# Kernel optimization log

Hardware: AMD Instinct MI355X
Metric: run time of the kernel (lower is better)

## Reference

```python
import jax, jax.numpy as jnp
import numpy as np

V, D, H, L, FF, C = 32000, 512, 8, 3, 2048, 6
B, S = 32, 1024


def setup_inputs() -> dict:
    key = jax.random.key(0)
    ks = jax.random.split(key, 8)
    tokens = jax.random.randint(ks[0], (B, S), 0, V, dtype=jnp.int32)
    emb = jax.random.normal(ks[1], (V, D), dtype=jnp.float32) * 0.02
    qkv_w = jax.random.normal(ks[2], (L, D, 3 * D), dtype=jnp.float32) * (D ** -0.5)
    qkv_b = jnp.zeros((L, 3 * D), dtype=jnp.float32)
    fc_w = jax.random.normal(ks[3], (L, D, D), dtype=jnp.float32) * (D ** -0.5)
    fc_b = jnp.zeros((L, D), dtype=jnp.float32)
    gamma = jnp.ones((D,), dtype=jnp.float32)
    beta = jnp.zeros((D,), dtype=jnp.float32)
    fc1_w = jax.random.normal(ks[4], (D, FF), dtype=jnp.float32) * (D ** -0.5)
    fc1_b = jnp.zeros((FF,), dtype=jnp.float32)
    fc2_w = jax.random.normal(ks[5], (FF, C), dtype=jnp.float32) * (FF ** -0.5)
    fc2_b = jnp.zeros((C,), dtype=jnp.float32)
    return dict(tokens=tokens, emb=emb, qkv_w=qkv_w, qkv_b=qkv_b, fc_w=fc_w,
                fc_b=fc_b, gamma=gamma, beta=beta, fc1_w=fc1_w, fc1_b=fc1_b,
                fc2_w=fc2_w, fc2_b=fc2_b)


def _sinusoidal_pe(seq_len, dim):
    pos = jnp.arange(seq_len, dtype=jnp.float32)[:, None]
    div = jnp.exp(jnp.arange(0, dim, 2).astype(jnp.float32) * (-np.log(10000.0) / dim))
    pe = jnp.zeros((seq_len, dim), dtype=jnp.float32)
    pe = pe.at[:, 0::2].set(jnp.sin(pos * div))
    pe = pe.at[:, 1::2].set(jnp.cos(pos * div))
    return pe


def reference(tokens, emb, qkv_w, qkv_b, fc_w, fc_b, gamma, beta, fc1_w, fc1_b, fc2_w, fc2_b):
    b, s = tokens.shape
    dh = D // H
    scale = dh ** -0.5

    def layernorm(y):
        m = y.mean(-1, keepdims=True)
        v = ((y - m) ** 2).mean(-1, keepdims=True)
        return (y - m) * jax.lax.rsqrt(v + 1e-5) * gamma + beta

    x = emb[tokens] + _sinusoidal_pe(s, D)[None]  # [B,S,D]
    for l in range(L):
        qkv = (x @ qkv_w[l] + qkv_b[l]).reshape(b, s, H, 3, dh)
        q = qkv[..., 0, :].transpose(0, 2, 1, 3)  # [B,H,S,dh]
        k = qkv[..., 1, :].transpose(0, 2, 1, 3)
        v = qkv[..., 2, :].transpose(0, 2, 1, 3)
        attn = jax.nn.softmax(jnp.einsum('bhqd,bhkd->bhqk', q, k) * scale, axis=-1)
        o = jnp.einsum('bhqk,bhkd->bhqd', attn, v).transpose(0, 2, 1, 3).reshape(b, s, D)
        o = o @ fc_w[l] + fc_b[l]
        x = layernorm(o + x)
    pooled = x.mean(axis=1)  # [B,D]
    h = jax.nn.relu(pooled @ fc1_w + fc1_b)  # dropout is identity at inference
    return h @ fc2_w + fc2_b
```

## Files before the change

### kernel.cpp

```cpp
#include <hip/hip_runtime.h>
#include <cmath>

#define BS_TOK 32768
#define DMODEL 512
#define NHEAD 8
#define DHEAD 64
#define NLAYER 3
#define FFDIM 2048
#define NCLS 6
#define BATCH 32
#define SEQ 1024
#define QKVW 1536

typedef short short8 __attribute__((ext_vector_type(8)));
typedef float float4v __attribute__((ext_vector_type(4)));
typedef unsigned int uint4v __attribute__((ext_vector_type(4)));
#define MFMA_BF16 __builtin_amdgcn_mfma_f32_16x16x32_bf16
#define QSCALE 0.18033688011112042f

__device__ __forceinline__ unsigned short f2bf(float x) {
    return (unsigned short)((__float_as_uint(x) + 0x8000u) >> 16);
}

__device__ __forceinline__ unsigned int cvt_pk_bf16(float a, float b) {
    unsigned int r;
    asm("v_cvt_pk_bf16_f32 %0, %1, %2" : "=v"(r) : "v"(a), "v"(b));
    return r;
}

#define PL32(a, b) asm("v_permlane32_swap_b32 %0, %1" : "+v"(a), "+v"(b))
#define PL16(a, b) asm("v_permlane16_swap_b32 %0, %1" : "+v"(a), "+v"(b))

__device__ __forceinline__ void gload16(const unsigned short* g, unsigned short* l) {
    __builtin_amdgcn_global_load_lds(
        (const __attribute__((address_space(1))) unsigned int*)g,
        (__attribute__((address_space(3))) unsigned int*)l, 16, 0, 0);
}

__global__ __launch_bounds__(128) void embed_pe_kernel(const int* __restrict__ tokens,
                                                       const float* __restrict__ emb,
                                                       float* __restrict__ X,
                                                       unsigned short* __restrict__ Xb) {
    int t = blockIdx.x;
    int pos = t & (SEQ - 1);
    int tok = tokens[t];
    int d0 = threadIdx.x * 4;
    float4 e = *(const float4*)(emb + (size_t)tok * DMODEL + d0);
    const float c = -9.210340371976184f / 512.0f;
    float div0 = expf((float)d0 * c);
    float div1 = expf((float)(d0 + 2) * c);
    float a0 = (float)pos * div0;
    float a1 = (float)pos * div1;
    e.x += sinf(a0); e.y += cosf(a0);
    e.z += sinf(a1); e.w += cosf(a1);
    *(float4*)(X + (size_t)t * DMODEL + d0) = e;
    *(ushort4*)(Xb + (size_t)t * DMODEL + d0) =
        make_ushort4(f2bf(e.x), f2bf(e.y), f2bf(e.z), f2bf(e.w));
}

__global__ __launch_bounds__(256) void transcvt_kernel(const float* __restrict__ in,
                                                       unsigned short* __restrict__ out,
                                                       int R, int C) {
    __shared__ float t[32][33];
    size_t base = (size_t)blockIdx.z * R * C;
    int c0 = blockIdx.x * 32, r0 = blockIdx.y * 32;
    int tx = threadIdx.x & 31, ty = threadIdx.x >> 5;
#pragma unroll
    for (int i = 0; i < 4; i++)
        t[ty + i * 8][tx] = in[base + (size_t)(r0 + ty + i * 8) * C + c0 + tx];
    __syncthreads();
#pragma unroll
    for (int i = 0; i < 4; i++)
        out[base + (size_t)(c0 + ty + i * 8) * R + r0 + tx] = f2bf(t[tx][ty + i * 8]);
}

__global__ __launch_bounds__(256) void transcvt_qkv_kernel(const float* __restrict__ in,
                                                           unsigned short* __restrict__ out) {
    __shared__ float t[32][33];
    int l = blockIdx.z;
    int n0 = blockIdx.x * 32, r0 = blockIdx.y * 32;
    int seg = n0 >> 9, nn = n0 & 511, h = nn >> 6, d0 = nn & 63;
    int c0 = h * 192 + seg * 64 + d0;
    float s = (seg == 0) ? QSCALE : 1.f;
    const float* inp = in + (size_t)l * DMODEL * QKVW;
    unsigned short* op = out + (size_t)l * QKVW * DMODEL;
    int tx = threadIdx.x & 31, ty = threadIdx.x >> 5;
#pragma unroll
    for (int i = 0; i < 4; i++)
        t[ty + i * 8][tx] = inp[(size_t)(r0 + ty + i * 8) * QKVW + c0 + tx];
    __syncthreads();
#pragma unroll
    for (int i = 0; i < 4; i++)
        op[(size_t)(n0 + ty + i * 8) * DMODEL + r0 + tx] = f2bf(t[tx][ty + i * 8] * s);
}

__global__ __launch_bounds__(256) void permbias_kernel(const float* __restrict__ qkv_b,
                                                       float* __restrict__ pb) {
    int i = blockIdx.x * 256 + threadIdx.x;
    int l = i / QKVW, n = i - l * QKVW;
    int seg = n >> 9, nn = n & 511, h = nn >> 6, d = nn & 63;
    float s = (seg == 0) ? QSCALE : 1.f;
    pb[i] = qkv_b[l * QKVW + h * 192 + seg * 64 + d] * s;
}

__global__ __launch_bounds__(256, 3) void gemm_qkv_kernel(const unsigned short* __restrict__ A,
                                                          const unsigned short* __restrict__ Bt,
                                                          const float* __restrict__ pb,
                                                          unsigned short* __restrict__ QKc,
                                                          unsigned short* __restrict__ Vt,
                                                          int M) {
    __shared__ unsigned short As[2][128 * 32];
    __shared__ unsigned short Bs[2][128 * 32];
    int bm = blockIdx.y * 128, bn = blockIdx.x * 128;
    int tid = threadIdx.x;
    int w = tid >> 6, lane = tid & 63, l15 = lane & 15, quad = lane >> 4;
    int wm = (w & 1) * 64, wn = (w >> 1) * 64;

    float4v acc[4][4];
    float4v z = {0.f, 0.f, 0.f, 0.f};
#pragma unroll
    for (int i = 0; i < 4; i++)
#pragma unroll
        for (int j = 0; j < 4; j++) acc[i][j] = z;

    int sr0 = w * 16 + (lane >> 2);
    int sr1 = (w + 4) * 16 + (lane >> 2);
    int sc = ((lane & 3) ^ ((lane >> 3) & 3)) * 8;
    const unsigned short* Ag = A + (size_t)bm * DMODEL;
    const unsigned short* Bg = Bt + (size_t)bn * DMODEL;

    gload16(Ag + (size_t)sr0 * DMODEL + sc, &As[0][w * 512]);
    gload16(Ag + (size_t)sr1 * DMODEL + sc, &As[0][(w + 4) * 512]);
    gload16(Bg + (size_t)sr0 * DMODEL + sc, &Bs[0][w * 512]);
    gload16(Bg + (size_t)sr1 * DMODEL + sc, &Bs[0][(w + 4) * 512]);
    __syncthreads();

    int sw = (l15 >> 1) & 3;
    for (int kt = 0; kt < 16; kt++) {
        const unsigned short* Ac = As[kt & 1];
        const unsigned short* Bc = Bs[kt & 1];
        if (kt + 1 < 16) {
            int kn = (kt + 1) * 32;
            unsigned short* An = (unsigned short*)As[(kt + 1) & 1];
            unsigned short* Bn = (unsigned short*)Bs[(kt + 1) & 1];
            gload16(Ag + (size_t)sr0 * DMODEL + kn + sc, &An[w * 512]);
            gload16(Ag + (size_t)sr1 * DMODEL + kn + sc, &An[(w + 4) * 512]);
            gload16(Bg + (size_t)sr0 * DMODEL + kn + sc, &Bn[w * 512]);
            gload16(Bg + (size_t)sr1 * DMODEL + kn + sc, &Bn[(w + 4) * 512]);
        }
        short8 af[4], bf[4];
#pragma unroll
        for (int i = 0; i < 4; i++)
            af[i] = *(short8*)&Ac[(wm + i * 16 + l15) * 32 + (quad ^ sw) * 8];
#pragma unroll
        for (int j = 0; j < 4; j++)
            bf[j] = *(short8*)&Bc[(wn + j * 16 + l15) * 32 + (quad ^ sw) * 8];
        __builtin_amdgcn_s_setprio(1);
#pragma unroll
        for (int i = 0; i < 4; i++)
#pragma unroll
            for (int j = 0; j < 4; j++)
                acc[i][j] = MFMA_BF16(af[i], bf[j], acc[i][j], 0, 0, 0);
        __builtin_amdgcn_s_setprio(0);
        __syncthreads();
    }

    float bj[4];
#pragma unroll
    for (int j = 0; j < 4; j++) bj[j] = pb[bn + wn + j * 16 + l15];

    if (bn < 1024) {
#pragma unroll
        for (int i = 0; i < 4; i++)
#pragma unroll
            for (int r = 0; r < 4; r++) {
                size_t row = (size_t)(bm + wm + i * 16 + quad * 4 + r);
#pragma unroll
                for (int j = 0; j < 4; j++)
                    QKc[row * 1024 + bn + wn + j * 16 + l15] = f2bf(acc[i][j][r] + bj[j]);
            }
    } else {
        int bl = bm >> 10;
        int sbase = (bm & 1023) + wm;
#pragma unroll
        for (int j = 0; j < 4; j++) {
            int colp = bn - 1024 + wn + j * 16 + l15;
            int h = colp >> 6, d = colp & 63;
            unsigned short* vb = Vt + ((size_t)(bl * 8 + h) * 64 + d) * 1024 + sbase;
#pragma unroll
            for (int i = 0; i < 4; i++) {
                ushort4 v4 = make_ushort4(f2bf(acc[i][j][0] + bj[j]),
                                          f2bf(acc[i][j][1] + bj[j]),
                                          f2bf(acc[i][j][2] + bj[j]),
                                          f2bf(acc[i][j][3] + bj[j]));
                *(ushort4*)(vb + i * 16 + quad * 4) = v4;
            }
        }
    }
}

__global__ __launch_bounds__(256, 2) void attn_kernel(const unsigned short* __restrict__ QKc,
                                                      const unsigned short* __restrict__ Vt,
                                                      unsigned short* __restrict__ O) {
    __shared__ unsigned short Ks[64 * 72];
    __shared__ unsigned short Vts[64 * 72];
    int bh = blockIdx.y;
    int b = bh >> 3, h = bh & 7;
    int q0 = blockIdx.x * 256;
    int tid = threadIdx.x;
    int w = tid >> 6, lane = tid & 63, l15 = lane & 15, quad = lane >> 4;
    const unsigned short* Kg = QKc + (size_t)b * SEQ * 1024 + 512 + h * 64;
    const unsigned short* Vg = Vt + (size_t)bh * 64 * 1024;

    short8 qf[4][2];
#pragma unroll
    for (int i = 0; i < 4; i++) {
        const unsigned short* qb =
            QKc + (size_t)(b * SEQ + q0 + w * 64 + i * 16 + l15) * 1024 + h * 64;
        qf[i][0] = *(const short8*)(qb + quad * 8);
        qf[i][1] = *(const short8*)(qb + 32 + quad * 8);
    }

    float lsum[4] = {0.f, 0.f, 0.f, 0.f};
    float4v accO[4][4];
    float4v z = {0.f, 0.f, 0.f, 0.f};
#pragma unroll
    for (int i = 0; i < 4; i++)
#pragma unroll
        for (int dc = 0; dc < 4; dc++) accO[i][dc] = z;

    int sr = tid >> 2, so = (tid & 3) * 16;

    short8 kp0, kp1, vp0, vp1;
    {
        const unsigned short* kg = Kg + (size_t)sr * 1024 + so;
        kp0 = *(const short8*)kg;
        kp1 = *(const short8*)(kg + 8);
        const unsigned short* vg = Vg + (size_t)sr * 1024 + so;
        vp0 = *(const short8*)vg;
        vp1 = *(const short8*)(vg + 8);
    }

    for (int jt = 0; jt < SEQ / 64; jt++) {
        __syncthreads();
        *(short8*)&Ks[sr * 72 + so] = kp0;
        *(short8*)&Ks[sr * 72 + so + 8] = kp1;
        *(short8*)&Vts[sr * 72 + so] = vp0;
        *(short8*)&Vts[sr * 72 + so + 8] = vp1;
        __syncthreads();

        if (jt + 1 < SEQ / 64) {
            const unsigned short* kg = Kg + (size_t)((jt + 1) * 64 + sr) * 1024 + so;
            kp0 = *(const short8*)kg;
            kp1 = *(const short8*)(kg + 8);
            const unsigned short* vg = Vg + (size_t)sr * 1024 + (jt + 1) * 64 + so;
            vp0 = *(const short8*)vg;
            vp1 = *(const short8*)(vg + 8);
        }

        short8 pa[4][2];
#pragma unroll
        for (int f = 0; f < 2; f++) {
            float4v st[4][2];
#pragma unroll
            for (int jj = 0; jj < 2; jj++) {
                int jc = f * 2 + jj;
                short8 kf0 = *(short8*)&Ks[(jc * 16 + l15) * 72 + quad * 8];
                short8 kf1 = *(short8*)&Ks[(jc * 16 + l15) * 72 + 32 + quad * 8];
#pragma unroll
                for (int i = 0; i < 4; i++) {
                    float4v s0 = MFMA_BF16(kf0, qf[i][0], z, 0, 0, 0);
                    st[i][jj] = MFMA_BF16(kf1, qf[i][1], s0, 0, 0, 0);
                }
            }
#pragma unroll
            for (int i = 0; i < 4; i++) {
                unsigned int pk[4];
#pragma unroll
                for (int jj = 0; jj < 2; jj++) {
                    float p0 = exp2f(st[i][jj][0]);
                    float p1 = exp2f(st[i][jj][1]);
                    float p2 = exp2f(st[i][jj][2]);
                    float p3 = exp2f(st[i][jj][3]);
                    lsum[i] += (p0 + p1) + (p2 + p3);
                    pk[jj * 2 + 0] = cvt_pk_bf16(p0, p1);
                    pk[jj * 2 + 1] = cvt_pk_bf16(p2, p3);
                }
                PL32(pk[0], pk[2]);
                PL32(pk[1], pk[3]);
                PL16(pk[0], pk[2]);
                PL16(pk[1], pk[3]);
                uint4v t;
                t[0] = pk[0]; t[1] = pk[1]; t[2] = pk[2]; t[3] = pk[3];
                pa[i][f] = __builtin_bit_cast(short8, t);
            }
        }

        __builtin_amdgcn_s_setprio(1);
#pragma unroll
        for (int dc = 0; dc < 4; dc++) {
            short8 vf0 = *(short8*)&Vts[(dc * 16 + l15) * 72 + quad * 8];
            short8 vf1 = *(short8*)&Vts[(dc * 16 + l15) * 72 + 32 + quad * 8];
#pragma unroll
            for (int i = 0; i < 4; i++) {
                accO[i][dc] = MFMA_BF16(pa[i][0], vf0, accO[i][dc], 0, 0, 0);
                accO[i][dc] = MFMA_BF16(pa[i][1], vf1, accO[i][dc], 0, 0, 0);
            }
        }
        __builtin_amdgcn_s_setprio(0);
    }

#pragma unroll
    for (int i = 0; i < 4; i++) {
        float s = lsum[i];
        s += __shfl_xor(s, 16);
        s += __shfl_xor(s, 32);
#pragma unroll
        for (int r = 0; r < 4; r++) {
            float rinv = 1.f / __shfl(s, quad * 4 + r);
            size_t row = (size_t)(b * SEQ + q0 + w * 64 + i * 16 + quad * 4 + r);
#pragma unroll
            for (int dc = 0; dc < 4; dc++)
                O[row * DMODEL + h * DHEAD + dc * 16 + l15] = f2bf(accO[i][dc][r] * rinv);
        }
    }
}

__global__ __launch_bounds__(256, 2) void proj_ln_kernel(const unsigned short* __restrict__ A,
                                                         const unsigned short* __restrict__ Bt,
                                                         const float* __restrict__ bias,
                                                         const float* __restrict__ gamma,
                                                         const float* __restrict__ beta,
                                                         float* __restrict__ X,
                                                         unsigned short* __restrict__ Xb) {
    __shared__ unsigned short As2[2][32 * 32];
    __shared__ unsigned short Bs2[2][512 * 32];
    __shared__ float redS[4][32], redQ[4][32];
    int bm = blockIdx.x * 32;
    int tid = threadIdx.x;
    int w = tid >> 6, lane = tid & 63, l15 = lane & 15, quad = lane >> 4;
    int wn = w * 128;

    float4v acc[2][8];
    float4v z = {0.f, 0.f, 0.f, 0.f};
#pragma unroll
    for (int i = 0; i < 2; i++)
#pragma unroll
        for (int j = 0; j < 8; j++) acc[i][j] = z;

    int lrow4 = lane >> 2;
    int sc = ((lane & 3) ^ ((lane >> 3) & 3)) * 8;
    const unsigned short* Ag = A + (size_t)bm * DMODEL;

    if (w < 2)
        gload16(Ag + (size_t)(w * 16 + lrow4) * DMODEL + sc, &As2[0][w * 512]);
#pragma unroll
    for (int u = 0; u < 8; u++) {
        int ch = w * 8 + u;
        gload16(Bt + (size_t)(ch * 16 + lrow4) * DMODEL + sc, &Bs2[0][ch * 512]);
    }
    __syncthreads();

    int sw = (l15 >> 1) & 3;
    for (int kt = 0; kt < 16; kt++) {
        const unsigned short* Ac = As2[kt & 1];
        const unsigned short* Bc = Bs2[kt & 1];
        if (kt + 1 < 16) {
            int kn = (kt + 1) * 32;
            unsigned short* An = (unsigned short*)As2[(kt + 1) & 1];
            unsigned short* Bn = (unsigned short*)Bs2[(kt + 1) & 1];
            if (w < 2)
                gload16(Ag + (size_t)(w * 16 + lrow4) * DMODEL + kn + sc, &An[w * 512]);
#pragma unroll
            for (int u = 0; u < 8; u++) {
                int ch = w * 8 + u;
                gload16(Bt + (size_t)(ch * 16 + lrow4) * DMODEL + kn + sc, &Bn[ch * 512]);
            }
        }
        short8 af[2];
#pragma unroll
        for (int i = 0; i < 2; i++)
            af[i] = *(short8*)&Ac[(i * 16 + l15) * 32 + (quad ^ sw) * 8];
        __builtin_amdgcn_s_setprio(1);
#pragma unroll
        for (int j = 0; j < 8; j++) {
            short8 bf = *(short8*)&Bc[(wn + j * 16 + l15) * 32 + (quad ^ sw) * 8];
            acc[0][j] = MFMA_BF16(af[0], bf, acc[0][j], 0, 0, 0);
            acc[1][j] = MFMA_BF16(af[1], bf, acc[1][j], 0, 0, 0);
        }
        __builtin_amdgcn_s_setprio(0);
        __syncthreads();
    }

    float bj[8], g[8], be[8];
#pragma unroll
    for (int j = 0; j < 8; j++) {
        int col = wn + j * 16 + l15;
        bj[j] = bias[col]; g[j] = gamma[col]; be[j] = beta[col];
    }

    float o[2][4][8];
#pragma unroll
    for (int i = 0; i < 2; i++)
#pragma unroll
        for (int r = 0; r < 4; r++) {
            int lrow = i * 16 + quad * 4 + r;
            size_t row = (size_t)(bm + lrow);
            float ss = 0.f, qq = 0.f;
#pragma unroll
            for (int j = 0; j < 8; j++) {
                float v = acc[i][j][r] + bj[j] + X[row * DMODEL + wn + j * 16 + l15];
                o[i][r][j] = v; ss += v; qq += v * v;
            }
#pragma unroll
            for (int mask = 1; mask < 16; mask <<= 1) {
                ss += __shfl_xor(ss, mask);
                qq += __shfl_xor(qq, mask);
            }
            if (l15 == 0) { redS[w][lrow] = ss; redQ[w][lrow] = qq; }
        }
    __syncthreads();
#pragma unroll
    for (int i = 0; i < 2; i++)
#pragma unroll
        for (int r = 0; r < 4; r++) {
            int lrow = i * 16 + quad * 4 + r;
            float S = redS[0][lrow] + redS[1][lrow] + redS[2][lrow] + redS[3][lrow];
            float Q = redQ[0][lrow] + redQ[1][lrow] + redQ[2][lrow] + redQ[3][lrow];
            float mean = S * (1.f / 512.f);
            float var = Q * (1.f / 512.f) - mean * mean;
            float rstd = rsqrtf(var + 1e-5f);
            size_t row = (size_t)(bm + lrow);
#pragma unroll
            for (int j = 0; j < 8; j++) {
                float n = (o[i][r][j] - mean) * rstd * g[j] + be[j];
                X[row * DMODEL + wn + j * 16 + l15] = n;
                Xb[row * DMODEL + wn + j * 16 + l15] = f2bf(n);
            }
        }
}

__global__ __launch_bounds__(256) void zero_kernel(float* __restrict__ p) {
    p[blockIdx.x * 256 + threadIdx.x] = 0.f;
}
__global__ __launch_bounds__(128) void pool_kernel(const float* __restrict__ X,
                                                   float* __restrict__ pooled) {
    int b = blockIdx.x, ch = blockIdx.y;
    int d0 = threadIdx.x * 4;
    float4 acc = make_float4(0.f, 0.f, 0.f, 0.f);
    const float* base = X + (size_t)(b * SEQ + ch * 64) * DMODEL + d0;
    for (int s2 = 0; s2 < 64; s2++) {
        float4 v = *(const float4*)(base + (size_t)s2 * DMODEL);
        acc.x += v.x; acc.y += v.y; acc.z += v.z; acc.w += v.w;
    }
    atomicAdd(pooled + b * DMODEL + d0 + 0, acc.x);
    atomicAdd(pooled + b * DMODEL + d0 + 1, acc.y);
    atomicAdd(pooled + b * DMODEL + d0 + 2, acc.z);
    atomicAdd(pooled + b * DMODEL + d0 + 3, acc.w);
}

__global__ __launch_bounds__(256) void fc1_kernel(const float* __restrict__ pooled,
                                                  const float* __restrict__ fc1_w,
                                                  const float* __restrict__ fc1_b,
                                                  float* __restrict__ h) {
    __shared__ float p[DMODEL];
    int ffc = blockIdx.x, b = blockIdx.y;
    int tid = threadIdx.x;
    p[tid] = pooled[b * DMODEL + tid] * (1.f / 1024.f);
    p[tid + 256] = pooled[b * DMODEL + tid + 256] * (1.f / 1024.f);
    __syncthreads();
    int ff = ffc * 256 + tid;
    float acc = fc1_b[ff];
    for (int k = 0; k < DMODEL; k++) acc += p[k] * fc1_w[(size_t)k * FFDIM + ff];
    h[(size_t)b * FFDIM + ff] = fmaxf(acc, 0.f);
}

__global__ __launch_bounds__(256) void fc2_kernel(const float* __restrict__ h,
                                                  const float* __restrict__ fc2_w,
                                                  const float* __restrict__ fc2_b,
                                                  float* __restrict__ out) {
    __shared__ float red[NCLS][256];
    int b = blockIdx.x, tid = threadIdx.x;
    float a[NCLS];
#pragma unroll
    for (int c = 0; c < NCLS; c++) a[c] = 0.f;
    int k0 = tid * 8;
#pragma unroll
    for (int u = 0; u < 8; u++) {
        float hv = h[(size_t)b * FFDIM + k0 + u];
#pragma unroll
        for (int c = 0; c < NCLS; c++) a[c] += hv * fc2_w[(k0 + u) * NCLS + c];
    }
#pragma unroll
    for (int c = 0; c < NCLS; c++) red[c][tid] = a[c];
    __syncthreads();
    if (tid < NCLS) {
        float s = 0.f;
        for (int i = 0; i < 256; i++) s += red[tid][i];
        out[b * NCLS + tid] = s + fc2_b[tid];
    }
}

extern "C" void kernel_launch(void* const* d_in, const int* in_sizes, int n_in,
                              void* d_out, int out_size, void* d_ws, size_t ws_size,
                              hipStream_t stream) {
    const int* tokens = (const int*)d_in[0];
    const float* emb = (const float*)d_in[1];
    const float* qkv_w = (const float*)d_in[2];
    const float* qkv_b = (const float*)d_in[3];
    const float* fc_w = (const float*)d_in[4];
    const float* fc_b = (const float*)d_in[5];
    const float* gamma = (const float*)d_in[6];
    const float* beta = (const float*)d_in[7];
    const float* fc1_w = (const float*)d_in[8];
    const float* fc1_b = (const float*)d_in[9];
    const float* fc2_w = (const float*)d_in[10];
    const float* fc2_b = (const float*)d_in[11];
    float* out = (float*)d_out;

    char* p = (char*)d_ws;
    float* X = (float*)p;                         p += (size_t)BS_TOK * DMODEL * 4;
    unsigned short* Xb = (unsigned short*)p;      p += (size_t)BS_TOK * DMODEL * 2;
    float* pooled = (float*)p;                    p += (size_t)BATCH * DMODEL * 4;
    float* hbuf = (float*)p;                      p += (size_t)BATCH * FFDIM * 4;
    float* pb = (float*)p;                        p += (size_t)NLAYER * QKVW * 4;
    unsigned short* qkv_wbt = (unsigned short*)p; p += (size_t)NLAYER * QKVW * DMODEL * 2;
    unsigned short* fc_wt = (unsigned short*)p;   p += (size_t)NLAYER * DMODEL * DMODEL * 2;
    size_t fixed_bytes = (size_t)(p - (char*)d_ws);
    size_t per_batch = (size_t)SEQ * 1024 * 2 + (size_t)NHEAD * 64 * SEQ * 2
                     + (size_t)SEQ * DMODEL * 2;
    int chunkB = 1;
    for (int cb = 32; cb >= 1; cb >>= 1)
        if (fixed_bytes + (size_t)cb * per_batch <= ws_size) { chunkB = cb; break; }
    unsigned short* QKc = (unsigned short*)p;     p += (size_t)chunkB * SEQ * 1024 * 2;
    unsigned short* Vt = (unsigned short*)p;      p += (size_t)chunkB * NHEAD * 64 * SEQ * 2;
    unsigned short* Oc = (unsigned short*)p;
    int rows = chunkB * SEQ;
    int nchunks = BATCH / chunkB;

    embed_pe_kernel<<<BS_TOK, 128, 0, stream>>>(tokens, emb, X, Xb);
    permbias_kernel<<<NLAYER * QKVW / 256, 256, 0, stream>>>(qkv_b, pb);
    transcvt_qkv_kernel<<<dim3(QKVW / 32, DMODEL / 32, NLAYER), 256, 0, stream>>>(
        qkv_w, qkv_wbt);
    transcvt_kernel<<<dim3(DMODEL / 32, DMODEL / 32, NLAYER), 256, 0, stream>>>(
        fc_w, fc_wt, DMODEL, DMODEL);

    for (int l = 0; l < NLAYER; l++) {
        for (int c = 0; c < nchunks; c++) {
            unsigned short* Xbc = Xb + (size_t)c * rows * DMODEL;
            float* Xc = X + (size_t)c * rows * DMODEL;
            gemm_qkv_kernel<<<dim3(QKVW / 128, rows / 128), 256, 0, stream>>>(
                Xbc, qkv_wbt + (size_t)l * QKVW * DMODEL, pb + (size_t)l * QKVW,
                QKc, Vt, rows);
            attn_kernel<<<dim3(SEQ / 256, chunkB * NHEAD), 256, 0, stream>>>(QKc, Vt, Oc);
            proj_ln_kernel<<<rows / 32, 256, 0, stream>>>(
                Oc, fc_wt + (size_t)l * DMODEL * DMODEL, fc_b + (size_t)l * DMODEL,
                gamma, beta, Xc, Xbc);
        }
    }

    zero_kernel<<<BATCH * DMODEL / 256, 256, 0, stream>>>(pooled);
    pool_kernel<<<dim3(BATCH, 16), 128, 0, stream>>>(X, pooled);
    fc1_kernel<<<dim3(FFDIM / 256, BATCH), 256, 0, stream>>>(pooled, fc1_w, fc1_b, hbuf);
    fc2_kernel<<<BATCH, 256, 0, stream>>>(hbuf, fc2_w, fc2_b, out);
}
```

Before: 904.4 us.

## Double-buffer attention K/V tiles with direct global-to-LDS loads and MFMA row sums

Rewrites the attention kernel's K/V staging. Tiles now go into double-buffered, XOR-swizzled LDS through direct global-to-LDS loads (gload16) in place of register staging and padded rows, leaving one barrier per iteration. The softmax denominator is accumulated with an MFMA against a vector of bf16 ones, replacing the scalar sums and final shuffles. The PV product is interleaved per half-tile, and the launch bound rises to 3 blocks per CU. This costs extra MFMA work, more LDS per block, and register pressure under the tighter occupancy target.

```diff
diff --git a/kernel.cpp b/kernel.cpp
--- a/kernel.cpp
+++ b/kernel.cpp
@@ -199,11 +199,11 @@
     }
 }
 
-__global__ __launch_bounds__(256, 2) void attn_kernel(const unsigned short* __restrict__ QKc,
+__global__ __launch_bounds__(256, 3) void attn_kernel(const unsigned short* __restrict__ QKc,
                                                       const unsigned short* __restrict__ Vt,
                                                       unsigned short* __restrict__ O) {
-    __shared__ unsigned short Ks[64 * 72];
-    __shared__ unsigned short Vts[64 * 72];
+    __shared__ unsigned short Ks[2][64 * 64];
+    __shared__ unsigned short Vts[2][64 * 64];
     int bh = blockIdx.y;
     int b = bh >> 3, h = bh & 7;
     int q0 = blockIdx.x * 256;
@@ -221,68 +221,67 @@
         qf[i][1] = *(const short8*)(qb + 32 + quad * 8);
     }
 
-    float lsum[4] = {0.f, 0.f, 0.f, 0.f};
     float4v accO[4][4];
+    float4v accL[4];
     float4v z = {0.f, 0.f, 0.f, 0.f};
 #pragma unroll
-    for (int i = 0; i < 4; i++)
+    for (int i = 0; i < 4; i++) {
+        accL[i] = z;
 #pragma unroll
         for (int dc = 0; dc < 4; dc++) accO[i][dc] = z;
-
-    int sr = tid >> 2, so = (tid & 3) * 16;
-
-    short8 kp0, kp1, vp0, vp1;
-    {
-        const unsigned short* kg = Kg + (size_t)sr * 1024 + so;
-        kp0 = *(const short8*)kg;
-        kp1 = *(const short8*)(kg + 8);
-        const unsigned short* vg = Vg + (size_t)sr * 1024 + so;
-        vp0 = *(const short8*)vg;
-        vp1 = *(const short8*)(vg + 8);
-    }
-
-    for (int jt = 0; jt < SEQ / 64; jt++) {
-        __syncthreads();
-        *(short8*)&Ks[sr * 72 + so] = kp0;
-        *(short8*)&Ks[sr * 72 + so + 8] = kp1;
-        *(short8*)&Vts[sr * 72 + so] = vp0;
-        *(short8*)&Vts[sr * 72 + so + 8] = vp1;
-        __syncthreads();
-
-        if (jt + 1 < SEQ / 64) {
-            const unsigned short* kg = Kg + (size_t)((jt + 1) * 64 + sr) * 1024 + so;
-            kp0 = *(const short8*)kg;
-            kp1 = *(const short8*)(kg + 8);
-            const unsigned short* vg = Vg + (size_t)sr * 1024 + (jt + 1) * 64 + so;
-            vp0 = *(const short8*)vg;
-            vp1 = *(const short8*)(vg + 8);
-        }
-
-        short8 pa[4][2];
+    }
+
+    short8 ones;
+#pragma unroll
+    for (int e = 0; e < 8; e++) ones[e] = (short)0x3F80;
+
+    int sub = lane >> 3;
+    int srow0 = w * 16 + sub;
+    int srow1 = w * 16 + 8 + sub;
+    int lc = ((lane & 7) ^ sub) * 8;
+
+    gload16(Kg + (size_t)srow0 * 1024 + lc, &Ks[0][w * 1024]);
+    gload16(Kg + (size_t)srow1 * 1024 + lc, &Ks[0][w * 1024 + 512]);
+    gload16(Vg + (size_t)srow0 * 1024 + lc, &Vts[0][w * 1024]);
+    gload16(Vg + (size_t)srow1 * 1024 + lc, &Vts[0][w * 1024 + 512]);
+    __syncthreads();
+
+    int cK = (quad ^ (l15 & 7)) * 8;
+
+    const int NT = SEQ / 64;
+    for (int jt = 0; jt < NT; jt++) {
+        const unsigned short* Kc = Ks[jt & 1];
+        const unsigned short* Vc = Vts[jt & 1];
+        if (jt + 1 < NT) {
+            unsigned short* Kn = (unsigned short*)Ks[(jt + 1) & 1];
+            unsigned short* Vn = (unsigned short*)Vts[(jt + 1) & 1];
+            gload16(Kg + (size_t)((jt + 1) * 64 + srow0) * 1024 + lc, &Kn[w * 1024]);
+            gload16(Kg + (size_t)((jt + 1) * 64 + srow1) * 1024 + lc, &Kn[w * 1024 + 512]);
+            gload16(Vg + (size_t)srow0 * 1024 + (jt + 1) * 64 + lc, &Vn[w * 1024]);
+            gload16(Vg + (size_t)srow1 * 1024 + (jt + 1) * 64 + lc, &Vn[w * 1024 + 512]);
+        }
+
 #pragma unroll
         for (int f = 0; f < 2; f++) {
-            float4v st[4][2];
-#pragma unroll
-            for (int jj = 0; jj < 2; jj++) {
-                int jc = f * 2 + jj;
-                short8 kf0 = *(short8*)&Ks[(jc * 16 + l15) * 72 + quad * 8];
-                short8 kf1 = *(short8*)&Ks[(jc * 16 + l15) * 72 + 32 + quad * 8];
-#pragma unroll
-                for (int i = 0; i < 4; i++) {
+            short8 pa[4];
+#pragma unroll
+            for (int i = 0; i < 4; i++) {
+                float4v st[2];
+#pragma unroll
+                for (int jj = 0; jj < 2; jj++) {
+                    int row = (f * 2 + jj) * 16 + l15;
+                    short8 kf0 = *(short8*)&Kc[row * 64 + cK];
+                    short8 kf1 = *(short8*)&Kc[row * 64 + (cK ^ 32)];
                     float4v s0 = MFMA_BF16(kf0, qf[i][0], z, 0, 0, 0);
-                    st[i][jj] = MFMA_BF16(kf1, qf[i][1], s0, 0, 0, 0);
+                    st[jj] = MFMA_BF16(kf1, qf[i][1], s0, 0, 0, 0);
                 }
-            }
-#pragma unroll
-            for (int i = 0; i < 4; i++) {
                 unsigned int pk[4];
 #pragma unroll
                 for (int jj = 0; jj < 2; jj++) {
-                    float p0 = exp2f(st[i][jj][0]);
-                    float p1 = exp2f(st[i][jj][1]);
-                    float p2 = exp2f(st[i][jj][2]);
-                    float p3 = exp2f(st[i][jj][3]);
-                    lsum[i] += (p0 + p1) + (p2 + p3);
+                    float p0 = exp2f(st[jj][0]);
+                    float p1 = exp2f(st[jj][1]);
+                    float p2 = exp2f(st[jj][2]);
+                    float p3 = exp2f(st[jj][3]);
                     pk[jj * 2 + 0] = cvt_pk_bf16(p0, p1);
                     pk[jj * 2 + 1] = cvt_pk_bf16(p2, p3);
                 }
@@ -292,38 +291,35 @@
                 PL16(pk[1], pk[3]);
                 uint4v t;
                 t[0] = pk[0]; t[1] = pk[1]; t[2] = pk[2]; t[3] = pk[3];
-                pa[i][f] = __builtin_bit_cast(short8, t);
-            }
-        }
-
-        __builtin_amdgcn_s_setprio(1);
-#pragma unroll
-        for (int dc = 0; dc < 4; dc++) {
-            short8 vf0 = *(short8*)&Vts[(dc * 16 + l15) * 72 + quad * 8];
-            short8 vf1 = *(short8*)&Vts[(dc * 16 + l15) * 72 + 32 + quad * 8];
-#pragma unroll
-            for (int i = 0; i < 4; i++) {
-                accO[i][dc] = MFMA_BF16(pa[i][0], vf0, accO[i][dc], 0, 0, 0);
-                accO[i][dc] = MFMA_BF16(pa[i][1], vf1, accO[i][dc], 0, 0, 0);
-            }
-        }
-        __builtin_amdgcn_s_setprio(0);
-    }
-
-#pragma unroll
-    for (int i = 0; i < 4; i++) {
-        float s = lsum[i];
-        s += __shfl_xor(s, 16);
-        s += __shfl_xor(s, 32);
+                pa[i] = __builtin_bit_cast(short8, t);
+            }
+
+            __builtin_amdgcn_s_setprio(1);
+#pragma unroll
+            for (int dc = 0; dc < 4; dc++) {
+                short8 vf = *(short8*)&Vc[(dc * 16 + l15) * 64 + (cK ^ (f * 32))];
+#pragma unroll
+                for (int i = 0; i < 4; i++)
+                    accO[i][dc] = MFMA_BF16(pa[i], vf, accO[i][dc], 0, 0, 0);
+            }
+#pragma unroll
+            for (int i = 0; i < 4; i++)
+                accL[i] = MFMA_BF16(pa[i], ones, accL[i], 0, 0, 0);
+            __builtin_amdgcn_s_setprio(0);
+        }
+        __syncthreads();
+    }
+
+#pragma unroll
+    for (int i = 0; i < 4; i++)
 #pragma unroll
         for (int r = 0; r < 4; r++) {
-            float rinv = 1.f / __shfl(s, quad * 4 + r);
+            float rinv = 1.f / accL[i][r];
             size_t row = (size_t)(b * SEQ + q0 + w * 64 + i * 16 + quad * 4 + r);
 #pragma unroll
             for (int dc = 0; dc < 4; dc++)
                 O[row * DMODEL + h * DHEAD + dc * 16 + l15] = f2bf(accO[i][dc][r] * rinv);
         }
-    }
 }
 
 __global__ __launch_bounds__(256, 2) void proj_ln_kernel(const unsigned short* __restrict__ A,
```

After: 923.8 us. 2.1% more time.
